# Optimization experiments

Measured on AMD Instinct MI355X. Metric: run time of the kernel, lower is better.

Reference implementation:

```python
import jax, jax.numpy as jnp
import numpy as np

N_NODES = 100000


def _gcn_conv(x, edge_index, W, b, num_nodes):
    """PyG GCNConv: x' = D^{-1/2} (A + I) D^{-1/2} (x W) + b."""
    xl = x @ W  # [N, H]
    loop = jnp.arange(num_nodes)
    row = jnp.concatenate([edge_index[0], loop])  # source
    col = jnp.concatenate([edge_index[1], loop])  # target
    deg = jax.ops.segment_sum(jnp.ones_like(col, dtype=xl.dtype), col,
                              num_segments=num_nodes)
    dinv = jnp.where(deg > 0, jax.lax.rsqrt(deg), 0.0)
    norm = dinv[row] * dinv[col]  # [E + N]
    msgs = xl[row] * norm[:, None]  # gather + scale
    out = jax.ops.segment_sum(msgs, col, num_segments=num_nodes)
    return out + b


def setup_inputs() -> dict:
    key = jax.random.key(0)
    ks = jax.random.split(key, 6)
    N, E, D, H, O = N_NODES, 1600000, 128, 64, 1
    x = jax.random.normal(ks[0], (N, D), dtype=jnp.float32)
    edge_index = jax.random.randint(ks[1], (2, E), 0, N, dtype=jnp.int64)
    W1 = jax.random.normal(ks[2], (D, H), dtype=jnp.float32) / np.sqrt(D)
    b1 = jnp.zeros((H,), dtype=jnp.float32)
    W2 = jax.random.normal(ks[3], (H, H), dtype=jnp.float32) / np.sqrt(H)
    b2 = jnp.zeros((H,), dtype=jnp.float32)
    Wfc = jax.random.normal(ks[4], (H, O), dtype=jnp.float32) / np.sqrt(H)
    bfc = jnp.zeros((O,), dtype=jnp.float32)
    return {"x": x, "edge_index": edge_index, "W1": W1, "b1": b1,
            "W2": W2, "b2": b2, "Wfc": Wfc, "bfc": bfc}


def reference(x, edge_index, W1, b1, W2, b2, Wfc, bfc):
    N = x.shape[0]
    h = jax.nn.relu(_gcn_conv(x, edge_index, W1, b1, N))
    h = jax.nn.relu(_gcn_conv(h, edge_index, W2, b2, N))
    return jax.nn.sigmoid(h @ Wfc + bfc)  # [N, 1]
```

## Files before the change

kernel.cpp:

```cpp
#include <hip/hip_runtime.h>
#include <math.h>


typedef __attribute__((ext_vector_type(8))) short bf16x8;
typedef __attribute__((ext_vector_type(4))) float f32x4;
typedef __attribute__((ext_vector_type(2))) float f32x2;

#define CHUNKS 1024

__device__ __forceinline__ unsigned short f2bf(float f) {
    unsigned u = __float_as_uint(f);
    u += 0x7FFFu + ((u >> 16) & 1u);
    return (unsigned short)(u >> 16);
}
__device__ __forceinline__ unsigned packbf(float a, float b) {
    return (unsigned)f2bf(a) | ((unsigned)f2bf(b) << 16);
}
__device__ __forceinline__ void upadd2(uint4 g, f32x2* a) {
    a[0] += (f32x2){__uint_as_float(g.x << 16), __uint_as_float(g.x & 0xFFFF0000u)};
    a[1] += (f32x2){__uint_as_float(g.y << 16), __uint_as_float(g.y & 0xFFFF0000u)};
    a[2] += (f32x2){__uint_as_float(g.z << 16), __uint_as_float(g.z & 0xFFFF0000u)};
    a[3] += (f32x2){__uint_as_float(g.w << 16), __uint_as_float(g.w & 0xFFFF0000u)};
}

__global__ __launch_bounds__(256) void k_hist(const int* __restrict__ col, int E,
                                              int NBUK, int CH,
                                              int* __restrict__ hist_g) {
    __shared__ int h[256];
    for (int i = threadIdx.x; i < NBUK; i += 256) h[i] = 0;
    __syncthreads();
    int base = blockIdx.x * CH, hi = min(base + CH, E);
    for (int e = base + (int)threadIdx.x; e < hi; e += 256)
        atomicAdd(&h[col[e] >> 9], 1);
    __syncthreads();
    for (int i = threadIdx.x; i < NBUK; i += 256)
        hist_g[blockIdx.x * NBUK + i] = h[i];
}

__global__ __launch_bounds__(256) void k_colscan(const int* __restrict__ hist_g, int NBUK,
                                                 int* __restrict__ histOff,
                                                 int* __restrict__ bucketTotal) {
    __shared__ int s[256];
    const int b = blockIdx.x, t = threadIdx.x;
    int v[4], sum = 0;
#pragma unroll
    for (int j = 0; j < 4; ++j) {
        v[j] = hist_g[(t * 4 + j) * NBUK + b];
        sum += v[j];
    }
    s[t] = sum;
    __syncthreads();
    for (int off = 1; off < 256; off <<= 1) {
        int u = (t >= off) ? s[t - off] : 0;
        __syncthreads();
        s[t] += u;
        __syncthreads();
    }
    int run = s[t] - sum;
#pragma unroll
    for (int j = 0; j < 4; ++j) {
        histOff[b * CHUNKS + t * 4 + j] = run;
        run += v[j];
    }
    if (t == 255) bucketTotal[b] = run;
}

__global__ __launch_bounds__(256) void k_scan_tot(const int* __restrict__ bucketTotal,
                                                  int NBUK, int E, int N,
                                                  int* __restrict__ bucketBase,
                                                  int* __restrict__ row_off) {
    __shared__ int s[256];
    int t = threadIdx.x;
    int v = (t < NBUK) ? bucketTotal[t] : 0;
    s[t] = v;
    __syncthreads();
    for (int off = 1; off < 256; off <<= 1) {
        int u = (t >= off) ? s[t - off] : 0;
        __syncthreads();
        s[t] += u;
        __syncthreads();
    }
    if (t < NBUK) bucketBase[t] = s[t] - v;
    if (t == 0) row_off[N] = E;
}

__global__ __launch_bounds__(256) void k_scatter(const int* __restrict__ row,
                                                 const int* __restrict__ col, int E,
                                                 int NBUK, int CH,
                                                 const int* __restrict__ bucketBase,
                                                 const int* __restrict__ histOff,
                                                 unsigned* __restrict__ ebuf) {
    __shared__ int cur[256];
    for (int i = threadIdx.x; i < NBUK; i += 256)
        cur[i] = bucketBase[i] + histOff[i * CHUNKS + blockIdx.x];
    __syncthreads();
    int base = blockIdx.x * CH, hi = min(base + CH, E);
    for (int e = base + (int)threadIdx.x; e < hi; e += 256) {
        int d = col[e], src = row[e];
        int b = d >> 9;
        int pos = atomicAdd(&cur[b], 1);
        ebuf[pos] = ((unsigned)(d & 511) << 17) | (unsigned)src;
    }
}

__global__ __launch_bounds__(512) void k_bucket(const unsigned* __restrict__ ebuf,
                                                const int* __restrict__ bucketBase,
                                                const int* __restrict__ bucketTotal,
                                                int N,
                                                int* __restrict__ row_off,
                                                float* __restrict__ dinv,
                                                int* __restrict__ csr_src) {
    __shared__ int hc[512], of[512];
    const int bid = blockIdx.x, t = threadIdx.x;
    const int base = bucketBase[bid];
    const int cnt  = bucketTotal[bid];
    hc[t] = 0;
    __syncthreads();
    for (int i = t; i < cnt; i += 512)
        atomicAdd(&hc[ebuf[base + i] >> 17], 1);
    __syncthreads();
    int v = hc[t];
    of[t] = v;
    __syncthreads();
    for (int off = 1; off < 512; off <<= 1) {
        int u = (t >= off) ? of[t - off] : 0;
        __syncthreads();
        of[t] += u;
        __syncthreads();
    }
    int excl = of[t] - v;
    int node = bid * 512 + t;
    if (node < N) {
        row_off[node] = base + excl;
        dinv[node] = rsqrtf((float)(v + 1));
    }
    of[t] = excl;
    __syncthreads();
    for (int i = t; i < cnt; i += 512) {
        unsigned e = ebuf[base + i];
        int dl = (int)(e >> 17), src = (int)(e & 0x1FFFFu);
        int pos = atomicAdd(&of[dl], 1);
        csr_src[base + pos] = src;
    }
}

template <int K, bool BF16IN>
__global__ __launch_bounds__(256) void k_gemm_mfma(const void* __restrict__ xin,
                                                   const float* __restrict__ W,
                                                   const float* __restrict__ dinv,
                                                   unsigned short* __restrict__ out,
                                                   int N) {
    constexpr int KS = K + 8;
    __shared__ short sX[64 * KS];
    __shared__ short sW[64 * KS];
    const int tid = threadIdx.x;
    const int wv = tid >> 6, lane = tid & 63;
    const int q = lane >> 4, m = lane & 15;
    const int nb = blockIdx.x * 64;

    for (int i = tid; i < K * 64; i += 256) {
        int k = i >> 6, c = i & 63;
        sW[c * KS + k] = (short)f2bf(W[i]);
    }
    if (BF16IN) {
        const unsigned short* xb = (const unsigned short*)xin;
        for (int i = tid; i < 64 * (K / 8); i += 256) {
            int r = i / (K / 8), c8 = (i % (K / 8)) * 8;
            int node = nb + r;
            uint4 v = make_uint4(0u, 0u, 0u, 0u);
            if (node < N) v = *(const uint4*)(xb + (size_t)node * K + c8);
            *(uint4*)(&sX[r * KS + c8]) = v;
        }
    } else {
        const float* xf = (const float*)xin;
        for (int i = tid; i < 64 * (K / 8); i += 256) {
            int r = i / (K / 8), c8 = (i % (K / 8)) * 8;
            int node = nb + r;
            uint4 v = make_uint4(0u, 0u, 0u, 0u);
            if (node < N) {
                float4 lo = *(const float4*)(xf + (size_t)node * K + c8);
                float4 hi = *(const float4*)(xf + (size_t)node * K + c8 + 4);
                v.x = packbf(lo.x, lo.y);
                v.y = packbf(lo.z, lo.w);
                v.z = packbf(hi.x, hi.y);
                v.w = packbf(hi.z, hi.w);
            }
            *(uint4*)(&sX[r * KS + c8]) = v;
        }
    }
    __syncthreads();

    f32x4 acc[4] = {};
    const short* aRow = &sX[(wv * 16 + m) * KS + q * 8];
#pragma unroll
    for (int k0 = 0; k0 < K; k0 += 32) {
        bf16x8 a = *(const bf16x8*)(aRow + k0);
#pragma unroll
        for (int ft = 0; ft < 4; ++ft) {
            bf16x8 b = *(const bf16x8*)(&sW[(ft * 16 + m) * KS + k0 + q * 8]);
            acc[ft] = __builtin_amdgcn_mfma_f32_16x16x32_bf16(a, b, acc[ft], 0, 0, 0);
        }
    }
#pragma unroll
    for (int r = 0; r < 4; ++r) {
        int node = nb + wv * 16 + q * 4 + r;
        if (node < N) {
            float di = dinv[node];
#pragma unroll
            for (int ft = 0; ft < 4; ++ft)
                out[(size_t)node * 64 + ft * 16 + m] = f2bf(acc[ft][r] * di);
        }
    }
}

__global__ __launch_bounds__(256) void k_agg(const unsigned short* __restrict__ xl,
                                             const int* __restrict__ row_off,
                                             const int* __restrict__ csr_src,
                                             const float* __restrict__ dinv,
                                             const float* __restrict__ bias,
                                             unsigned short* __restrict__ out, int N) {
    const int wave = threadIdx.x >> 6, lane = threadIdx.x & 63;
    const int s = lane >> 3, o = lane & 7;
    int node = (blockIdx.x * 4 + wave) * 8 + s;
    const bool active = node < N;
    node = min(node, N - 1);
    const int beg = row_off[node];
    const int deg = row_off[node + 1] - beg;
    const int cnt = active ? deg + 1 : 0;
    int mx = cnt;
    mx = max(mx, __shfl_xor(mx, 8, 64));
    mx = max(mx, __shfl_xor(mx, 16, 64));
    mx = max(mx, __shfl_xor(mx, 32, 64));
    const char* xlb = (const char*)xl;
    const unsigned loff = (unsigned)(o << 4);
    f32x2 acc0[4] = {}, acc1[4] = {};
    int idx0 = (0 < deg) ? csr_src[beg] : node;
    int idx1 = (1 < deg) ? csr_src[beg + 1] : node;
    for (int it = 0; it < mx; it += 2) {
        const int c0 = idx0, c1 = idx1;
        const bool v0 = it < cnt, v1 = (it + 1) < cnt;
        idx0 = (it + 2 < deg) ? csr_src[beg + it + 2] : node;
        idx1 = (it + 3 < deg) ? csr_src[beg + it + 3] : node;
        uint4 g0 = *(const uint4*)(xlb + (((unsigned)c0 << 7) | loff));
        uint4 g1 = *(const uint4*)(xlb + (((unsigned)c1 << 7) | loff));
        if (!v0) g0 = make_uint4(0u, 0u, 0u, 0u);
        if (!v1) g1 = make_uint4(0u, 0u, 0u, 0u);
        upadd2(g0, acc0);
        upadd2(g1, acc1);
    }
#pragma unroll
    for (int j = 0; j < 4; ++j) acc0[j] += acc1[j];
    if (active) {
        float di = dinv[node];
        float4 blo = *(const float4*)(bias + o * 8);
        float4 bhi = *(const float4*)(bias + o * 8 + 4);
        uint4 r;
        r.x = packbf(fmaxf(acc0[0].x * di + blo.x, 0.f), fmaxf(acc0[0].y * di + blo.y, 0.f));
        r.y = packbf(fmaxf(acc0[1].x * di + blo.z, 0.f), fmaxf(acc0[1].y * di + blo.w, 0.f));
        r.z = packbf(fmaxf(acc0[2].x * di + bhi.x, 0.f), fmaxf(acc0[2].y * di + bhi.y, 0.f));
        r.w = packbf(fmaxf(acc0[3].x * di + bhi.z, 0.f), fmaxf(acc0[3].y * di + bhi.w, 0.f));
        *(uint4*)(out + (size_t)node * 64 + o * 8) = r;
    }
}

__global__ __launch_bounds__(256) void k_agg_fc(const unsigned short* __restrict__ xl,
                                                const int* __restrict__ row_off,
                                                const int* __restrict__ csr_src,
                                                const float* __restrict__ dinv,
                                                const float* __restrict__ bias,
                                                const float* __restrict__ Wfc,
                                                const float* __restrict__ bfc,
                                                float* __restrict__ out, int N) {
    const int wave = threadIdx.x >> 6, lane = threadIdx.x & 63;
    const int s = lane >> 3, o = lane & 7;
    int node = (blockIdx.x * 4 + wave) * 8 + s;
    const bool active = node < N;
    node = min(node, N - 1);
    const int beg = row_off[node];
    const int deg = row_off[node + 1] - beg;
    const int cnt = active ? deg + 1 : 0;
    int mx = cnt;
    mx = max(mx, __shfl_xor(mx, 8, 64));
    mx = max(mx, __shfl_xor(mx, 16, 64));
    mx = max(mx, __shfl_xor(mx, 32, 64));
    const char* xlb = (const char*)xl;
    const unsigned loff = (unsigned)(o << 4);
    f32x2 acc0[4] = {}, acc1[4] = {};
    int idx0 = (0 < deg) ? csr_src[beg] : node;
    int idx1 = (1 < deg) ? csr_src[beg + 1] : node;
    for (int it = 0; it < mx; it += 2) {
        const int c0 = idx0, c1 = idx1;
        const bool v0 = it < cnt, v1 = (it + 1) < cnt;
        idx0 = (it + 2 < deg) ? csr_src[beg + it + 2] : node;
        idx1 = (it + 3 < deg) ? csr_src[beg + it + 3] : node;
        uint4 g0 = *(const uint4*)(xlb + (((unsigned)c0 << 7) | loff));
        uint4 g1 = *(const uint4*)(xlb + (((unsigned)c1 << 7) | loff));
        if (!v0) g0 = make_uint4(0u, 0u, 0u, 0u);
        if (!v1) g1 = make_uint4(0u, 0u, 0u, 0u);
        upadd2(g0, acc0);
        upadd2(g1, acc1);
    }
#pragma unroll
    for (int j = 0; j < 4; ++j) acc0[j] += acc1[j];
    const float di = dinv[node];
    float4 blo = *(const float4*)(bias + o * 8);
    float4 bhi = *(const float4*)(bias + o * 8 + 4);
    float4 wlo = *(const float4*)(Wfc + o * 8);
    float4 whi = *(const float4*)(Wfc + o * 8 + 4);
    float v = 0.f;
    v += fmaxf(acc0[0].x * di + blo.x, 0.f) * wlo.x;
    v += fmaxf(acc0[0].y * di + blo.y, 0.f) * wlo.y;
    v += fmaxf(acc0[1].x * di + blo.z, 0.f) * wlo.z;
    v += fmaxf(acc0[1].y * di + blo.w, 0.f) * wlo.w;
    v += fmaxf(acc0[2].x * di + bhi.x, 0.f) * whi.x;
    v += fmaxf(acc0[2].y * di + bhi.y, 0.f) * whi.y;
    v += fmaxf(acc0[3].x * di + bhi.z, 0.f) * whi.z;
    v += fmaxf(acc0[3].y * di + bhi.w, 0.f) * whi.w;
    v += __shfl_xor(v, 1, 64);
    v += __shfl_xor(v, 2, 64);
    v += __shfl_xor(v, 4, 64);
    if (active && o == 0) out[node] = 1.f / (1.f + expf(-(v + bfc[0])));
}

extern "C" void kernel_launch(void* const* d_in, const int* in_sizes, int n_in,
                              void* d_out, int out_size, void* d_ws, size_t ws_size,
                              hipStream_t stream) {
    const float* x   = (const float*)d_in[0];
    const int*   ei  = (const int*)d_in[1];
    const float* W1  = (const float*)d_in[2];
    const float* b1  = (const float*)d_in[3];
    const float* W2  = (const float*)d_in[4];
    const float* b2  = (const float*)d_in[5];
    const float* Wfc = (const float*)d_in[6];
    const float* bfc = (const float*)d_in[7];
    float* out = (float*)d_out;

    const int H = in_sizes[3];
    const int D = in_sizes[2] / H;
    const int N = in_sizes[0] / D;
    const int E = in_sizes[1] / 2;
    const int* row = ei;
    const int* col = ei + E;
    const int NBUK = (N + 511) >> 9;
    const int CH   = (E + CHUNKS - 1) / CHUNKS;

    char* p = (char*)d_ws;
    auto carve = [&](size_t bytes) {
        char* r = p;
        p += (bytes + 255) & ~(size_t)255;
        return (void*)r;
    };
    int*            hist_g      = (int*)carve((size_t)CHUNKS * 256 * 4);
    int*            histOff     = (int*)carve((size_t)256 * CHUNKS * 4);
    int*            bucketTotal = (int*)carve((size_t)256 * 4);
    int*            bucketBase  = (int*)carve((size_t)256 * 4);
    unsigned*       ebuf        = (unsigned*)carve((size_t)E * 4);
    int*            csr_src     = (int*)carve((size_t)E * 4);
    int*            row_off     = (int*)carve((size_t)(N + 1) * 4);
    float*          dinv        = (float*)carve((size_t)N * 4);
    unsigned short* bufXL       = (unsigned short*)carve((size_t)N * 64 * 2);
    unsigned short* bufH        = (unsigned short*)carve((size_t)N * 64 * 2);
    (void)ws_size;

    const int TB = 256;
    k_hist<<<CHUNKS, TB, 0, stream>>>(col, E, NBUK, CH, hist_g);
    k_colscan<<<NBUK, TB, 0, stream>>>(hist_g, NBUK, histOff, bucketTotal);
    k_scan_tot<<<1, TB, 0, stream>>>(bucketTotal, NBUK, E, N, bucketBase, row_off);
    k_scatter<<<CHUNKS, TB, 0, stream>>>(row, col, E, NBUK, CH, bucketBase, histOff, ebuf);
    k_bucket<<<NBUK, 512, 0, stream>>>(ebuf, bucketBase, bucketTotal, N,
                                       row_off, dinv, csr_src);

    int gemmGrid = (N + 63) / 64;
    int aggGrid  = (N + 31) / 32;
    k_gemm_mfma<128, false><<<gemmGrid, TB, 0, stream>>>(x, W1, dinv, bufXL, N);
    k_agg<<<aggGrid, TB, 0, stream>>>(bufXL, row_off, csr_src, dinv, b1, bufH, N);
    k_gemm_mfma<64, true><<<gemmGrid, TB, 0, stream>>>(bufH, W2, dinv, bufXL, N);
    k_agg_fc<<<aggGrid, TB, 0, stream>>>(bufXL, row_off, csr_src, dinv, b2, Wfc, bfc, out, N);
}
```

Before: 223.2 us.

## Fuse layer-1 aggregation with layer-2 GEMM and unroll gathers by four

Merges the first aggregation kernel with the second-layer GEMM. Each wave writes its 8 aggregated rows to shared memory, pads them to a 16-row tile, and runs MFMA against W2 converted to bf16 in LDS. This removes one kernel launch and a round trip of the hidden features through global memory. Both aggregation loops also move from 2 to 4 outstanding gathers per iteration to expose more memory-level parallelism. In exchange, every block reconverts W2 into LDS, half of each MFMA tile is wasted padding, and register use goes up.

Measured after the change: 217.3 us. 2.7% less time.

```diff
diff --git a/kernel.cpp b/kernel.cpp
--- a/kernel.cpp
+++ b/kernel.cpp
@@ -213,15 +213,32 @@
     }
 }
 
-__global__ __launch_bounds__(256) void k_agg(const unsigned short* __restrict__ xl,
-                                             const int* __restrict__ row_off,
-                                             const int* __restrict__ csr_src,
-                                             const float* __restrict__ dinv,
-                                             const float* __restrict__ bias,
-                                             unsigned short* __restrict__ out, int N) {
-    const int wave = threadIdx.x >> 6, lane = threadIdx.x & 63;
+__global__ __launch_bounds__(256) void k_agg_g2(const unsigned short* __restrict__ xl,
+                                                const int* __restrict__ row_off,
+                                                const int* __restrict__ csr_src,
+                                                const float* __restrict__ dinv,
+                                                const float* __restrict__ bias,
+                                                const float* __restrict__ W2,
+                                                unsigned short* __restrict__ out, int N) {
+    constexpr int KS = 72;
+    __shared__ short sH[4 * 16 * KS];
+    __shared__ short sW2[64 * KS];
+    const int tid = threadIdx.x;
+    const int wv = tid >> 6, lane = tid & 63;
     const int s = lane >> 3, o = lane & 7;
-    int node = (blockIdx.x * 4 + wave) * 8 + s;
+    const int q = lane >> 4, m = lane & 15;
+
+    for (int i = tid; i < 64 * 64; i += 256) {
+        int k = i >> 6, n = i & 63;
+        sW2[n * KS + k] = (short)f2bf(W2[i]);
+    }
+    short* myH = &sH[wv * 16 * KS];
+    for (int i = lane; i < 8 * KS / 4; i += 64)
+        ((unsigned long long*)(myH + 8 * KS))[i] = 0ull;
+    __syncthreads();
+
+    const int base8 = (blockIdx.x * 4 + wv) * 8;
+    int node = base8 + s;
     const bool active = node < N;
     node = min(node, N - 1);
     const int beg = row_off[node];
@@ -234,32 +251,65 @@
     const char* xlb = (const char*)xl;
     const unsigned loff = (unsigned)(o << 4);
     f32x2 acc0[4] = {}, acc1[4] = {};
-    int idx0 = (0 < deg) ? csr_src[beg] : node;
-    int idx1 = (1 < deg) ? csr_src[beg + 1] : node;
-    for (int it = 0; it < mx; it += 2) {
-        const int c0 = idx0, c1 = idx1;
-        const bool v0 = it < cnt, v1 = (it + 1) < cnt;
-        idx0 = (it + 2 < deg) ? csr_src[beg + it + 2] : node;
-        idx1 = (it + 3 < deg) ? csr_src[beg + it + 3] : node;
-        uint4 g0 = *(const uint4*)(xlb + (((unsigned)c0 << 7) | loff));
-        uint4 g1 = *(const uint4*)(xlb + (((unsigned)c1 << 7) | loff));
-        if (!v0) g0 = make_uint4(0u, 0u, 0u, 0u);
-        if (!v1) g1 = make_uint4(0u, 0u, 0u, 0u);
+    int idx[4];
+#pragma unroll
+    for (int j = 0; j < 4; ++j) idx[j] = (j < deg) ? csr_src[beg + j] : node;
+    for (int it = 0; it < mx; it += 4) {
+        int c[4];
+        bool v[4];
+#pragma unroll
+        for (int j = 0; j < 4; ++j) {
+            c[j] = idx[j];
+            v[j] = (it + j) < cnt;
+            idx[j] = (it + 4 + j < deg) ? csr_src[beg + it + 4 + j] : node;
+        }
+        uint4 g0 = *(const uint4*)(xlb + (((unsigned)c[0] << 7) | loff));
+        uint4 g1 = *(const uint4*)(xlb + (((unsigned)c[1] << 7) | loff));
+        uint4 g2 = *(const uint4*)(xlb + (((unsigned)c[2] << 7) | loff));
+        uint4 g3 = *(const uint4*)(xlb + (((unsigned)c[3] << 7) | loff));
+        if (!v[0]) g0 = make_uint4(0u, 0u, 0u, 0u);
+        if (!v[1]) g1 = make_uint4(0u, 0u, 0u, 0u);
+        if (!v[2]) g2 = make_uint4(0u, 0u, 0u, 0u);
+        if (!v[3]) g3 = make_uint4(0u, 0u, 0u, 0u);
         upadd2(g0, acc0);
         upadd2(g1, acc1);
+        upadd2(g2, acc0);
+        upadd2(g3, acc1);
     }
 #pragma unroll
     for (int j = 0; j < 4; ++j) acc0[j] += acc1[j];
-    if (active) {
+    {
         float di = dinv[node];
         float4 blo = *(const float4*)(bias + o * 8);
         float4 bhi = *(const float4*)(bias + o * 8 + 4);
-        uint4 r;
-        r.x = packbf(fmaxf(acc0[0].x * di + blo.x, 0.f), fmaxf(acc0[0].y * di + blo.y, 0.f));
-        r.y = packbf(fmaxf(acc0[1].x * di + blo.z, 0.f), fmaxf(acc0[1].y * di + blo.w, 0.f));
-        r.z = packbf(fmaxf(acc0[2].x * di + bhi.x, 0.f), fmaxf(acc0[2].y * di + bhi.y, 0.f));
-        r.w = packbf(fmaxf(acc0[3].x * di + bhi.z, 0.f), fmaxf(acc0[3].y * di + bhi.w, 0.f));
-        *(uint4*)(out + (size_t)node * 64 + o * 8) = r;
+        uint4 h;
+        h.x = packbf(fmaxf(acc0[0].x * di + blo.x, 0.f), fmaxf(acc0[0].y * di + blo.y, 0.f));
+        h.y = packbf(fmaxf(acc0[1].x * di + blo.z, 0.f), fmaxf(acc0[1].y * di + blo.w, 0.f));
+        h.z = packbf(fmaxf(acc0[2].x * di + bhi.x, 0.f), fmaxf(acc0[2].y * di + bhi.y, 0.f));
+        h.w = packbf(fmaxf(acc0[3].x * di + bhi.z, 0.f), fmaxf(acc0[3].y * di + bhi.w, 0.f));
+        *(uint4*)(myH + s * KS + o * 8) = h;
+    }
+    f32x4 accm[4] = {};
+#pragma unroll
+    for (int k0 = 0; k0 < 64; k0 += 32) {
+        bf16x8 a = *(const bf16x8*)(myH + m * KS + q * 8 + k0);
+#pragma unroll
+        for (int ft = 0; ft < 4; ++ft) {
+            bf16x8 b = *(const bf16x8*)(&sW2[(ft * 16 + m) * KS + k0 + q * 8]);
+            accm[ft] = __builtin_amdgcn_mfma_f32_16x16x32_bf16(a, b, accm[ft], 0, 0, 0);
+        }
+    }
+    if (q < 2) {
+#pragma unroll
+        for (int r = 0; r < 4; ++r) {
+            int node2 = base8 + q * 4 + r;
+            if (node2 < N) {
+                float di2 = dinv[node2];
+#pragma unroll
+                for (int ft = 0; ft < 4; ++ft)
+                    out[(size_t)node2 * 64 + ft * 16 + m] = f2bf(accm[ft][r] * di2);
+            }
+        }
     }
 }
 
@@ -286,19 +336,30 @@
     const char* xlb = (const char*)xl;
     const unsigned loff = (unsigned)(o << 4);
     f32x2 acc0[4] = {}, acc1[4] = {};
-    int idx0 = (0 < deg) ? csr_src[beg] : node;
-    int idx1 = (1 < deg) ? csr_src[beg + 1] : node;
-    for (int it = 0; it < mx; it += 2) {
-        const int c0 = idx0, c1 = idx1;
-        const bool v0 = it < cnt, v1 = (it + 1) < cnt;
-        idx0 = (it + 2 < deg) ? csr_src[beg + it + 2] : node;
-        idx1 = (it + 3 < deg) ? csr_src[beg + it + 3] : node;
-        uint4 g0 = *(const uint4*)(xlb + (((unsigned)c0 << 7) | loff));
-        uint4 g1 = *(const uint4*)(xlb + (((unsigned)c1 << 7) | loff));
-        if (!v0) g0 = make_uint4(0u, 0u, 0u, 0u);
-        if (!v1) g1 = make_uint4(0u, 0u, 0u, 0u);
+    int idx[4];
+#pragma unroll
+    for (int j = 0; j < 4; ++j) idx[j] = (j < deg) ? csr_src[beg + j] : node;
+    for (int it = 0; it < mx; it += 4) {
+        int c[4];
+        bool v[4];
+#pragma unroll
+        for (int j = 0; j < 4; ++j) {
+            c[j] = idx[j];
+            v[j] = (it + j) < cnt;
+            idx[j] = (it + 4 + j < deg) ? csr_src[beg + it + 4 + j] : node;
+        }
+        uint4 g0 = *(const uint4*)(xlb + (((unsigned)c[0] << 7) | loff));
+        uint4 g1 = *(const uint4*)(xlb + (((unsigned)c[1] << 7) | loff));
+        uint4 g2 = *(const uint4*)(xlb + (((unsigned)c[2] << 7) | loff));
+        uint4 g3 = *(const uint4*)(xlb + (((unsigned)c[3] << 7) | loff));
+        if (!v[0]) g0 = make_uint4(0u, 0u, 0u, 0u);
+        if (!v[1]) g1 = make_uint4(0u, 0u, 0u, 0u);
+        if (!v[2]) g2 = make_uint4(0u, 0u, 0u, 0u);
+        if (!v[3]) g3 = make_uint4(0u, 0u, 0u, 0u);
         upadd2(g0, acc0);
         upadd2(g1, acc1);
+        upadd2(g2, acc0);
+        upadd2(g3, acc1);
     }
 #pragma unroll
     for (int j = 0; j < 4; ++j) acc0[j] += acc1[j];
@@ -359,7 +420,7 @@
     int*            row_off     = (int*)carve((size_t)(N + 1) * 4);
     float*          dinv        = (float*)carve((size_t)N * 4);
     unsigned short* bufXL       = (unsigned short*)carve((size_t)N * 64 * 2);
-    unsigned short* bufH        = (unsigned short*)carve((size_t)N * 64 * 2);
+    unsigned short* bufXL2      = (unsigned short*)carve((size_t)N * 64 * 2);
     (void)ws_size;
 
     const int TB = 256;
@@ -373,7 +434,6 @@
     int gemmGrid = (N + 63) / 64;
     int aggGrid  = (N + 31) / 32;
     k_gemm_mfma<128, false><<<gemmGrid, TB, 0, stream>>>(x, W1, dinv, bufXL, N);
-    k_agg<<<aggGrid, TB, 0, stream>>>(bufXL, row_off, csr_src, dinv, b1, bufH, N);
-    k_gemm_mfma<64, true><<<gemmGrid, TB, 0, stream>>>(bufH, W2, dinv, bufXL, N);
-    k_agg_fc<<<aggGrid, TB, 0, stream>>>(bufXL, row_off, csr_src, dinv, b2, Wfc, bfc, out, N);
-}
+    k_agg_g2<<<aggGrid, TB, 0, stream>>>(bufXL, row_off, csr_src, dinv, b1, W2, bufXL2, N);
+    k_agg_fc<<<aggGrid, TB, 0, stream>>>(bufXL2, row_off, csr_src, dinv, b2, Wfc, bfc, out, N);
+}
```
